# Optimization experiments

Measured on AMD Instinct MI355X. Metric: run time of the kernel, lower is better.

## Reference

```python
import jax, jax.numpy as jnp
import numpy as np

BETA = 0.2
ALPHA_NEG = 0.8
ALPHA_POS = 0.2
EPS = 1e-8  # torch cosine_similarity eps

B, D, P = 8192, 256, 4096


def setup_inputs() -> dict:
    key = jax.random.key(0)
    k1, k2 = jax.random.split(key)
    embeddings = jax.random.normal(k1, (B, D), dtype=jnp.float32)
    positive_pairs = jax.random.randint(k2, (P, 2), 0, B, dtype=jnp.int32)
    return {"embeddings": embeddings, "positive_pairs": positive_pairs}


def reference(embeddings, positive_pairs):
    b = embeddings.shape[0]
    p = positive_pairs.shape[0]
    # cosine similarity matrix (normalize once, single GEMM)
    nrm = jnp.maximum(jnp.linalg.norm(embeddings, axis=1, keepdims=True), EPS)
    e = embeddings / nrm
    cos = e @ e.T                              # [B, B]
    exp_cos = jnp.exp(cos / BETA)
    ii = positive_pairs[:, 0]
    jj = positive_pairs[:, 1]
    # mask = eye + positive pairs (both directions)
    mask = jnp.eye(b, dtype=bool)
    mask = mask.at[ii, jj].set(True).at[jj, ii].set(True)
    exp_masked = jnp.where(mask, 0.0, exp_cos)  # masked_fill(mask, 0)
    pos_ij = exp_cos[ii, jj]                   # [P]
    pos_ji = exp_cos[jj, ii]                   # [P]
    exp_i = exp_masked[ii]                     # [P, B]
    exp_j = exp_masked[jj]                     # [P, B]
    # hard-negative mining via alpha_neg quantile per row
    thr_i = jnp.quantile(exp_i, ALPHA_NEG, axis=1, keepdims=True)
    thr_j = jnp.quantile(exp_j, ALPHA_NEG, axis=1, keepdims=True)
    S_i = jnp.sum(jnp.where(exp_i >= thr_i, exp_i, 0.0), axis=1)  # [P]
    S_j = jnp.sum(jnp.where(exp_j >= thr_j, exp_j, 0.0), axis=1)  # [P]
    # hard-positive mining via alpha_pos quantile
    thr_pij = jnp.quantile(pos_ij, ALPHA_POS)
    thr_pji = jnp.quantile(pos_ji, ALPHA_POS)
    sel_ij = pos_ij <= thr_pij
    sel_ji = pos_ji <= thr_pji
    # torch loop zips the two (order-preserving) boolean-selected lists ->
    # truncates to min count; values are never cross-coupled, only the count.
    kmin = jnp.minimum(sel_ij.sum(), sel_ji.sum())
    act_ij = sel_ij & ((jnp.cumsum(sel_ij.astype(jnp.int32)) - 1) < kmin)
    act_ji = sel_ji & ((jnp.cumsum(sel_ji.astype(jnp.int32)) - 1) < kmin)
    # -log(pk / (pk + S[m])) = log1p(S[m] / pk), summed over all m per pk
    term_ij = jnp.log1p(S_i[None, :] / pos_ij[:, None])  # [P, P]
    term_ji = jnp.log1p(S_j[None, :] / pos_ji[:, None])  # [P, P]
    loss = (jnp.sum(term_ij * act_ij[:, None].astype(term_ij.dtype))
            + jnp.sum(term_ji * act_ji[:, None].astype(term_ji.dtype)))
    return loss / (2.0 * p)
```

## Files before the change

### kernel.cpp

```cpp
#include <hip/hip_runtime.h>
#include <stdint.h>

#define BN    8192
#define DK    256
#define PN    4096
#define MAXP  16
#define HBASE 0x340
#define RANK_ASC 6553

typedef __bf16  bf16_8 __attribute__((ext_vector_type(8)));
typedef __bf16  bf16_4 __attribute__((ext_vector_type(4)));
typedef float   f32x4  __attribute__((ext_vector_type(4)));

__device__ __forceinline__ void gload_lds16(const void* g, void* l) {
  __builtin_amdgcn_global_load_lds(
      (const __attribute__((address_space(1))) unsigned int*)g,
      (__attribute__((address_space(3))) unsigned int*)l, 16, 0, 0);
}

__global__ void prep_clear_kernel(int* pcount, int* rowlist, int* cnt, float* acc) {
  const int i = blockIdx.x * 256 + threadIdx.x;
  if (i < BN) { pcount[i] = 0; rowlist[i] = 0; }
  if (i < 8) acc[i] = 0.f;
  if (i == 0) cnt[0] = 0;
}

__global__ void prep_pairs_kernel(const int2* __restrict__ pairs,
                                  int* pcount, int* partners) {
  const int p = blockIdx.x * 256 + threadIdx.x;
  if (p >= PN) return;
  int2 pr = pairs[p];
  int ix = atomicAdd(&pcount[pr.x], 1);
  if (ix < MAXP) partners[pr.x * MAXP + ix] = pr.y;
  int iy = atomicAdd(&pcount[pr.y], 1);
  if (iy < MAXP) partners[pr.y * MAXP + iy] = pr.x;
}

__global__ void prep_compact_kernel(const int* __restrict__ pcount,
                                    int* rowlist, int* cnt) {
  const int i = blockIdx.x * 256 + threadIdx.x;
  if (i < BN && pcount[i] > 0) {
    int pos = atomicAdd(cnt, 1);
    rowlist[pos] = i;
  }
}

__global__ void __launch_bounds__(256) normalize_kernel(
    const float* __restrict__ X, float* __restrict__ E, __bf16* __restrict__ Ebf) {
  const int tid  = threadIdx.x;
  const int lane = tid & 63;
  const int w    = tid >> 6;
  const int row  = blockIdx.x * 4 + w;
  float4 x = ((const float4*)(X + (size_t)row * DK))[lane];
  float ss = x.x * x.x + x.y * x.y + x.z * x.z + x.w * x.w;
  #pragma unroll
  for (int o = 32; o; o >>= 1) ss += __shfl_xor(ss, o);
  float nrm = fmaxf(sqrtf(ss), 1e-8f);
  float4 e;
  e.x = x.x / nrm; e.y = x.y / nrm; e.z = x.z / nrm; e.w = x.w / nrm;
  ((float4*)(E + (size_t)row * DK))[lane] = e;
  bf16_4 b;
  b[0] = (__bf16)e.x; b[1] = (__bf16)e.y; b[2] = (__bf16)e.z; b[3] = (__bf16)e.w;
  *(bf16_4*)(Ebf + (size_t)row * DK + lane * 4) = b;
}

__global__ void __launch_bounds__(256) pos_kernel(
    const float* __restrict__ E, const int2* __restrict__ pairs, float* __restrict__ pos) {
  const int tid  = threadIdx.x;
  const int lane = tid & 63;
  const int w    = tid >> 6;
  const int p    = blockIdx.x * 4 + w;
  int2 pr = pairs[p];
  float4 a = ((const float4*)(E + (size_t)pr.x * DK))[lane];
  float4 b = ((const float4*)(E + (size_t)pr.y * DK))[lane];
  float d = a.x * b.x + a.y * b.y + a.z * b.z + a.w * b.w;
  #pragma unroll
  for (int o = 32; o; o >>= 1) d += __shfl_xor(d, o);
  if (lane == 0) pos[p] = __expf(5.0f * d);
}

__device__ __forceinline__ void find_bin_256(const unsigned* hist, int rank,
                                             int* sh, unsigned* wtot) {
  const int tid = threadIdx.x, lane = tid & 63, w = tid >> 6;
  unsigned x = hist[tid];
  unsigned pref = x;
  #pragma unroll
  for (int o = 1; o < 64; o <<= 1) {
    unsigned y = __shfl_up(pref, o);
    if (lane >= o) pref += y;
  }
  if (lane == 63) wtot[w] = pref;
  __syncthreads();
  unsigned woff = 0;
  for (int i = 0; i < w; ++i) woff += wtot[i];
  unsigned incl = pref + woff, excl = incl - x;
  if ((unsigned)rank >= excl && (unsigned)rank < incl) { sh[0] = tid; sh[1] = rank - (int)excl; }
  __syncthreads();
}

__global__ void __launch_bounds__(256) pos_thr_kernel(
    const float* __restrict__ pos, float* __restrict__ thr_out) {
  __shared__ uint32_t v[PN];
  __shared__ unsigned hist[256];
  __shared__ int sh[2];
  __shared__ unsigned wtot[4];
  const int tid = threadIdx.x;
  for (int i = tid; i < PN; i += 256) v[i] = ((const uint32_t*)pos)[i];
  __syncthreads();
  int rank = 819;
  uint32_t prefix = 0;
  for (int pass = 0; pass < 4; ++pass) {
    const int shift = 24 - pass * 8;
    hist[tid] = 0;
    __syncthreads();
    for (int i = tid; i < PN; i += 256) {
      uint32_t x = v[i];
      bool match = (pass == 0) || ((x >> (shift + 8)) == (prefix >> (shift + 8)));
      if (match) atomicAdd(&hist[(x >> shift) & 255u], 1u);
    }
    __syncthreads();
    find_bin_256(hist, rank, sh, wtot);
    prefix |= ((uint32_t)sh[0]) << shift;
    rank = sh[1];
    __syncthreads();
  }
  if (tid == 0) {
    float f;
    __builtin_memcpy(&f, &prefix, 4);
    thr_out[0] = f;
  }
}

__global__ void __launch_bounds__(256) gemm_exp_kernel(
    const __bf16* __restrict__ E, const int* __restrict__ rowlist,
    const int* __restrict__ countp, _Float16* __restrict__ out) {
  if ((int)blockIdx.y * 128 >= *countp) return;
  __shared__ __align__(16) __bf16 sA[128 * 32];
  __shared__ __align__(16) __bf16 sB[128 * 32];
  const int tid  = threadIdx.x;
  const int lane = tid & 63;
  const int w    = tid >> 6;
  const int wm   = w >> 1, wn = w & 1;
  const int trow = blockIdx.y * 128;
  const int tcol = blockIdx.x * 128;
  const int r0   = tid >> 2;
  const int seg  = tid & 3;

  const int ga0 = rowlist[trow + r0];
  const int ga1 = rowlist[trow + 64 + r0];
  const __bf16* pa0 = E + (size_t)ga0 * DK + seg * 8;
  const __bf16* pa1 = E + (size_t)ga1 * DK + seg * 8;
  const __bf16* pb0 = E + (size_t)(tcol + r0) * DK + seg * 8;
  const __bf16* pb1 = E + (size_t)(tcol + 64 + r0) * DK + seg * 8;
  __bf16* la0 = &sA[tid * 8];
  __bf16* la1 = &sA[2048 + tid * 8];
  __bf16* lb0 = &sB[tid * 8];
  __bf16* lb1 = &sB[2048 + tid * 8];

  f32x4 acc[4][4];
  #pragma unroll
  for (int i = 0; i < 4; ++i)
    #pragma unroll
    for (int j = 0; j < 4; ++j) {
      f32x4 z = {0.f, 0.f, 0.f, 0.f};
      acc[i][j] = z;
    }

  for (int kt = 0; kt < 8; ++kt) {
    const int k0 = kt * 32;
    __syncthreads();
    gload_lds16(pa0 + k0, la0);
    gload_lds16(pa1 + k0, la1);
    gload_lds16(pb0 + k0, lb0);
    gload_lds16(pb1 + k0, lb1);
    __syncthreads();
    bf16_8 af[4], bfg[4];
    #pragma unroll
    for (int t = 0; t < 4; ++t) {
      af[t]  = *(const bf16_8*)&sA[(wm * 64 + t * 16 + (lane & 15)) * 32 + (lane >> 4) * 8];
      bfg[t] = *(const bf16_8*)&sB[(wn * 64 + t * 16 + (lane & 15)) * 32 + (lane >> 4) * 8];
    }
    #pragma unroll
    for (int i = 0; i < 4; ++i)
      #pragma unroll
      for (int j = 0; j < 4; ++j)
        acc[i][j] = __builtin_amdgcn_mfma_f32_16x16x32_bf16(af[i], bfg[j], acc[i][j], 0, 0, 0);
  }

  const int crow = trow + wm * 64 + (lane >> 4) * 4;
  const int ccol = tcol + wn * 64 + (lane & 15);
  #pragma unroll
  for (int i = 0; i < 4; ++i)
    #pragma unroll
    for (int j = 0; j < 4; ++j)
      #pragma unroll
      for (int r = 0; r < 4; ++r) {
        const int row = crow + i * 16 + r;
        const int col = ccol + j * 16;
        out[(size_t)row * BN + col] = (_Float16)__expf(acc[i][j][r] * 5.0f);
      }
}

__global__ void __launch_bounds__(256) row_stats_kernel(
    const _Float16* __restrict__ expmat, const int* __restrict__ rowlist,
    const int* __restrict__ countp, const int* __restrict__ pcount,
    const int* __restrict__ partners, float* __restrict__ S) {
  __shared__ unsigned hist[4][256];
  __shared__ unsigned total[256];
  __shared__ int plist[MAXP + 1];
  __shared__ int sh[2];
  __shared__ unsigned wtot[4];
  __shared__ float redf[2][4];
  __shared__ unsigned redc[4];
  const int rloc = blockIdx.x;
  if (rloc >= *countp) return;
  const int grow = rowlist[rloc];
  const int tid = threadIdx.x, lane = tid & 63, w = tid >> 6;

  uint4 rv[4];
  const uint4* src = (const uint4*)(expmat + (size_t)rloc * BN);
  #pragma unroll
  for (int q = 0; q < 4; ++q) rv[q] = src[q * 256 + tid];

  int np = pcount[grow]; if (np > MAXP) np = MAXP;
  if (tid < np) plist[tid] = partners[grow * MAXP + tid];
  if (tid == np) plist[tid] = grow;
  ((unsigned*)hist)[tid]       = 0;
  ((unsigned*)hist)[tid + 256] = 0;
  ((unsigned*)hist)[tid + 512] = 0;
  ((unsigned*)hist)[tid + 768] = 0;
  __syncthreads();

  unsigned short hv[32];
  #pragma unroll
  for (int q = 0; q < 4; ++q) {
    union { uint4 u; unsigned short s[8]; } cv;
    cv.u = rv[q];
    #pragma unroll
    for (int j = 0; j < 8; ++j) hv[q * 8 + j] = cv.s[j];
  }

  for (int e = 0; e <= np; ++e) {
    int c = plist[e];
    if (((c >> 3) & 255) == tid) hv[((c >> 11) << 3) | (c & 7)] = 0;
  }

  unsigned* h = hist[w];
  #pragma unroll
  for (int e = 0; e < 32; ++e) {
    int bb = (int)(hv[e] >> 4) - HBASE;
    bb = bb < 0 ? 0 : (bb > 255 ? 255 : bb);
    atomicAdd(&h[bb], 1u);
  }
  __syncthreads();
  total[tid] = hist[0][tid] + hist[1][tid] + hist[2][tid] + hist[3][tid];
  __syncthreads();
  find_bin_256(total, RANK_ASC, sh, wtot);
  const int b    = sh[0];
  const int need = (int)total[b] - sh[1];

  float shi = 0.f, sin_ = 0.f; unsigned cin = 0;
  #pragma unroll
  for (int e = 0; e < 32; ++e) {
    unsigned short x = hv[e];
    int bb = (int)(x >> 4) - HBASE;
    bb = bb < 0 ? 0 : (bb > 255 ? 255 : bb);
    _Float16 hf; __builtin_memcpy(&hf, &x, 2);
    float v = (float)hf;
    if (bb > b) shi += v;
    else if (bb == b) { sin_ += v; cin++; }
  }
  #pragma unroll
  for (int o = 32; o; o >>= 1) {
    shi  += __shfl_xor(shi, o);
    sin_ += __shfl_xor(sin_, o);
    cin  += __shfl_xor(cin, o);
  }
  if (lane == 0) { redf[0][w] = shi; redf[1][w] = sin_; redc[w] = cin; }
  __syncthreads();
  if (tid == 0) {
    float SHI = redf[0][0] + redf[0][1] + redf[0][2] + redf[0][3];
    float SIN = redf[1][0] + redf[1][1] + redf[1][2] + redf[1][3];
    float CIN = (float)(redc[0] + redc[1] + redc[2] + redc[3]);
    S[grow] = SHI + (float)need * (SIN / CIN);
  }
}

__global__ void __launch_bounds__(256) pair_terms_kernel(
    const int2* __restrict__ pairs, const float* __restrict__ S,
    float* __restrict__ acc) {
  __shared__ float red[3][4];
  const int tid = threadIdx.x, lane = tid & 63, w = tid >> 6;
  float t = 0.f, u = 0.f, v = 0.f;
  for (int c = tid; c < PN; c += 256) {
    int2 pr = pairs[c];
    float s1 = S[pr.x], s2 = S[pr.y];
    float i1 = 1.f / s1, i2 = 1.f / s2;
    t += __logf(s1) + __logf(s2);
    u += i1 + i2;
    v += i1 * i1 + i2 * i2;
  }
  #pragma unroll
  for (int o = 32; o; o >>= 1) {
    t += __shfl_xor(t, o); u += __shfl_xor(u, o); v += __shfl_xor(v, o);
  }
  if (lane == 0) { red[0][w] = t; red[1][w] = u; red[2][w] = v; }
  __syncthreads();
  if (tid == 0) {
    acc[0] = red[0][0] + red[0][1] + red[0][2] + red[0][3];
    acc[1] = red[1][0] + red[1][1] + red[1][2] + red[1][3];
    acc[2] = red[2][0] + red[2][1] + red[2][2] + red[2][3];
  }
}

__global__ void __launch_bounds__(256) active_sums_kernel(
    const float* __restrict__ pos, const float* __restrict__ thr_p,
    float* __restrict__ acc) {
  __shared__ float red[4][4];
  const int tid = threadIdx.x, lane = tid & 63, w = tid >> 6;
  const float thr = thr_p[0];
  float n = 0.f, sl = 0.f, sp = 0.f, sp2 = 0.f;
  for (int r = tid; r < PN; r += 256) {
    float p = pos[r];
    if (p <= thr) { n += 1.f; sl += __logf(p); sp += p; sp2 += p * p; }
  }
  #pragma unroll
  for (int o = 32; o; o >>= 1) {
    n += __shfl_xor(n, o); sl += __shfl_xor(sl, o);
    sp += __shfl_xor(sp, o); sp2 += __shfl_xor(sp2, o);
  }
  if (lane == 0) { red[0][w] = n; red[1][w] = sl; red[2][w] = sp; red[3][w] = sp2; }
  __syncthreads();
  if (tid == 0) {
    acc[3] = red[0][0] + red[0][1] + red[0][2] + red[0][3];
    acc[4] = red[1][0] + red[1][1] + red[1][2] + red[1][3];
    acc[5] = red[2][0] + red[2][1] + red[2][2] + red[2][3];
    acc[6] = red[3][0] + red[3][1] + red[3][2] + red[3][3];
  }
}

__global__ void final_loss_kernel(const float* __restrict__ acc, float* __restrict__ out) {
  double T = acc[0], U = acc[1], V = acc[2];
  double n = acc[3], sl = acc[4], sp = acc[5], sp2 = acc[6];
  double num = n * T - 2.0 * (double)PN * sl + sp * U - 0.5 * sp2 * V;
  out[0] = (float)(num / (2.0 * (double)PN));
}

extern "C" void kernel_launch(void* const* d_in, const int* in_sizes, int n_in,
                              void* d_out, int out_size, void* d_ws, size_t ws_size,
                              hipStream_t stream) {
  const float* emb  = (const float*)d_in[0];
  const int2* pairs = (const int2*)d_in[1];
  float* out = (float*)d_out;

  char* w = (char*)d_ws;
  size_t off = 0;
  float*    E     = (float*)(w + off);    off += (size_t)BN * DK * 4;
  __bf16*   Ebf   = (__bf16*)(w + off);   off += (size_t)BN * DK * 2;
  float*    S     = (float*)(w + off);    off += (size_t)BN * 4;
  float*    pos   = (float*)(w + off);    off += (size_t)PN * 4;
  float*    thrp  = (float*)(w + off);    off += 256;
  float*    acc   = (float*)(w + off);    off += 256;
  int*      pcnt  = (int*)(w + off);      off += (size_t)BN * 4;
  int*      parts = (int*)(w + off);      off += (size_t)BN * MAXP * 4;
  int*      rlist = (int*)(w + off);      off += (size_t)BN * 4;
  int*      cnt   = (int*)(w + off);      off += 256;
  _Float16* expc  = (_Float16*)(w + off); off += (size_t)BN * BN * 2;

  prep_clear_kernel<<<BN / 256, 256, 0, stream>>>(pcnt, rlist, cnt, acc);
  normalize_kernel<<<BN / 4, 256, 0, stream>>>(emb, E, Ebf);
  prep_pairs_kernel<<<PN / 256, 256, 0, stream>>>(pairs, pcnt, parts);
  prep_compact_kernel<<<BN / 256, 256, 0, stream>>>(pcnt, rlist, cnt);
  pos_kernel<<<PN / 4, 256, 0, stream>>>(E, pairs, pos);
  pos_thr_kernel<<<1, 256, 0, stream>>>(pos, thrp);
  gemm_exp_kernel<<<dim3(BN / 128, BN / 128), 256, 0, stream>>>(Ebf, rlist, cnt, expc);
  row_stats_kernel<<<BN, 256, 0, stream>>>(expc, rlist, cnt, pcnt, parts, S);
  pair_terms_kernel<<<1, 256, 0, stream>>>(pairs, S, acc);
  active_sums_kernel<<<1, 256, 0, stream>>>(pos, thrp, acc);
  final_loss_kernel<<<1, 1, 0, stream>>>(acc, out);
}
```

Measured before the change: 171.7 us.

## Store exp matrix as fp8 packed by row groups, histogram directly on bytes

```diff
diff --git a/kernel.cpp b/kernel.cpp
--- a/kernel.cpp
+++ b/kernel.cpp
@@ -5,7 +5,6 @@
 #define DK    256
 #define PN    4096
 #define MAXP  16
-#define HBASE 0x340
 #define RANK_ASC 6553
 
 typedef __bf16  bf16_8 __attribute__((ext_vector_type(8)));
@@ -18,10 +17,9 @@
       (__attribute__((address_space(3))) unsigned int*)l, 16, 0, 0);
 }
 
-__global__ void prep_clear_kernel(int* pcount, int* rowlist, int* cnt, float* acc) {
+__global__ void prep_clear_kernel(int* pcount, int* rowlist, int* cnt) {
   const int i = blockIdx.x * 256 + threadIdx.x;
   if (i < BN) { pcount[i] = 0; rowlist[i] = 0; }
-  if (i < 8) acc[i] = 0.f;
   if (i == 0) cnt[0] = 0;
 }
 
@@ -98,42 +96,9 @@
   __syncthreads();
 }
 
-__global__ void __launch_bounds__(256) pos_thr_kernel(
-    const float* __restrict__ pos, float* __restrict__ thr_out) {
-  __shared__ uint32_t v[PN];
-  __shared__ unsigned hist[256];
-  __shared__ int sh[2];
-  __shared__ unsigned wtot[4];
-  const int tid = threadIdx.x;
-  for (int i = tid; i < PN; i += 256) v[i] = ((const uint32_t*)pos)[i];
-  __syncthreads();
-  int rank = 819;
-  uint32_t prefix = 0;
-  for (int pass = 0; pass < 4; ++pass) {
-    const int shift = 24 - pass * 8;
-    hist[tid] = 0;
-    __syncthreads();
-    for (int i = tid; i < PN; i += 256) {
-      uint32_t x = v[i];
-      bool match = (pass == 0) || ((x >> (shift + 8)) == (prefix >> (shift + 8)));
-      if (match) atomicAdd(&hist[(x >> shift) & 255u], 1u);
-    }
-    __syncthreads();
-    find_bin_256(hist, rank, sh, wtot);
-    prefix |= ((uint32_t)sh[0]) << shift;
-    rank = sh[1];
-    __syncthreads();
-  }
-  if (tid == 0) {
-    float f;
-    __builtin_memcpy(&f, &prefix, 4);
-    thr_out[0] = f;
-  }
-}
-
 __global__ void __launch_bounds__(256) gemm_exp_kernel(
     const __bf16* __restrict__ E, const int* __restrict__ rowlist,
-    const int* __restrict__ countp, _Float16* __restrict__ out) {
+    const int* __restrict__ countp, uint32_t* __restrict__ out4) {
   if ((int)blockIdx.y * 128 >= *countp) return;
   __shared__ __align__(16) __bf16 sA[128 * 32];
   __shared__ __align__(16) __bf16 sB[128 * 32];
@@ -190,160 +155,179 @@
   const int crow = trow + wm * 64 + (lane >> 4) * 4;
   const int ccol = tcol + wn * 64 + (lane & 15);
   #pragma unroll
-  for (int i = 0; i < 4; ++i)
-    #pragma unroll
-    for (int j = 0; j < 4; ++j)
-      #pragma unroll
-      for (int r = 0; r < 4; ++r) {
-        const int row = crow + i * 16 + r;
-        const int col = ccol + j * 16;
-        out[(size_t)row * BN + col] = (_Float16)__expf(acc[i][j][r] * 5.0f);
-      }
-}
-
-__global__ void __launch_bounds__(256) row_stats_kernel(
-    const _Float16* __restrict__ expmat, const int* __restrict__ rowlist,
+  for (int i = 0; i < 4; ++i) {
+    const int gidx = (crow + i * 16) >> 2;
+    #pragma unroll
+    for (int j = 0; j < 4; ++j) {
+      const int col = ccol + j * 16;
+      float e0 = __expf(acc[i][j][0] * 5.0f);
+      float e1 = __expf(acc[i][j][1] * 5.0f);
+      float e2 = __expf(acc[i][j][2] * 5.0f);
+      float e3 = __expf(acc[i][j][3] * 5.0f);
+      int u = __builtin_amdgcn_cvt_pk_fp8_f32(e0, e1, 0, false);
+      u     = __builtin_amdgcn_cvt_pk_fp8_f32(e2, e3, u, true);
+      out4[(size_t)gidx * BN + col] = (uint32_t)u;
+    }
+  }
+}
+
+__global__ void __launch_bounds__(256) row_stats4_kernel(
+    const uint32_t* __restrict__ expc4, const int* __restrict__ rowlist,
     const int* __restrict__ countp, const int* __restrict__ pcount,
     const int* __restrict__ partners, float* __restrict__ S) {
-  __shared__ unsigned hist[4][256];
-  __shared__ unsigned total[256];
-  __shared__ int plist[MAXP + 1];
+  __shared__ unsigned hist[4][4][256];
+  __shared__ unsigned total[4][256];
+  __shared__ int plist[4][MAXP + 1];
+  __shared__ int npl[4];
+  __shared__ int growl[4];
   __shared__ int sh[2];
   __shared__ unsigned wtot[4];
-  __shared__ float redf[2][4];
-  __shared__ unsigned redc[4];
-  const int rloc = blockIdx.x;
-  if (rloc >= *countp) return;
-  const int grow = rowlist[rloc];
+  __shared__ float redf[4];
+  const int g = blockIdx.x;
+  const int cnt = *countp;
+  if (g * 4 >= cnt) return;
   const int tid = threadIdx.x, lane = tid & 63, w = tid >> 6;
 
-  uint4 rv[4];
-  const uint4* src = (const uint4*)(expmat + (size_t)rloc * BN);
-  #pragma unroll
-  for (int q = 0; q < 4; ++q) rv[q] = src[q * 256 + tid];
-
-  int np = pcount[grow]; if (np > MAXP) np = MAXP;
-  if (tid < np) plist[tid] = partners[grow * MAXP + tid];
-  if (tid == np) plist[tid] = grow;
-  ((unsigned*)hist)[tid]       = 0;
-  ((unsigned*)hist)[tid + 256] = 0;
-  ((unsigned*)hist)[tid + 512] = 0;
-  ((unsigned*)hist)[tid + 768] = 0;
-  __syncthreads();
-
-  unsigned short hv[32];
-  #pragma unroll
-  for (int q = 0; q < 4; ++q) {
-    union { uint4 u; unsigned short s[8]; } cv;
-    cv.u = rv[q];
-    #pragma unroll
-    for (int j = 0; j < 8; ++j) hv[q * 8 + j] = cv.s[j];
-  }
-
-  for (int e = 0; e <= np; ++e) {
-    int c = plist[e];
-    if (((c >> 3) & 255) == tid) hv[((c >> 11) << 3) | (c & 7)] = 0;
-  }
-
-  unsigned* h = hist[w];
-  #pragma unroll
-  for (int e = 0; e < 32; ++e) {
-    int bb = (int)(hv[e] >> 4) - HBASE;
-    bb = bb < 0 ? 0 : (bb > 255 ? 255 : bb);
-    atomicAdd(&h[bb], 1u);
-  }
-  __syncthreads();
-  total[tid] = hist[0][tid] + hist[1][tid] + hist[2][tid] + hist[3][tid];
-  __syncthreads();
-  find_bin_256(total, RANK_ASC, sh, wtot);
-  const int b    = sh[0];
-  const int need = (int)total[b] - sh[1];
-
-  float shi = 0.f, sin_ = 0.f; unsigned cin = 0;
-  #pragma unroll
-  for (int e = 0; e < 32; ++e) {
-    unsigned short x = hv[e];
-    int bb = (int)(x >> 4) - HBASE;
-    bb = bb < 0 ? 0 : (bb > 255 ? 255 : bb);
-    _Float16 hf; __builtin_memcpy(&hf, &x, 2);
-    float v = (float)hf;
-    if (bb > b) shi += v;
-    else if (bb == b) { sin_ += v; cin++; }
-  }
-  #pragma unroll
-  for (int o = 32; o; o >>= 1) {
-    shi  += __shfl_xor(shi, o);
-    sin_ += __shfl_xor(sin_, o);
-    cin  += __shfl_xor(cin, o);
-  }
-  if (lane == 0) { redf[0][w] = shi; redf[1][w] = sin_; redc[w] = cin; }
-  __syncthreads();
-  if (tid == 0) {
-    float SHI = redf[0][0] + redf[0][1] + redf[0][2] + redf[0][3];
-    float SIN = redf[1][0] + redf[1][1] + redf[1][2] + redf[1][3];
-    float CIN = (float)(redc[0] + redc[1] + redc[2] + redc[3]);
-    S[grow] = SHI + (float)need * (SIN / CIN);
-  }
-}
-
-__global__ void __launch_bounds__(256) pair_terms_kernel(
-    const int2* __restrict__ pairs, const float* __restrict__ S,
-    float* __restrict__ acc) {
-  __shared__ float red[3][4];
-  const int tid = threadIdx.x, lane = tid & 63, w = tid >> 6;
-  float t = 0.f, u = 0.f, v = 0.f;
+  uint4 rv[8];
+  const uint4* src = (const uint4*)(expc4 + (size_t)g * BN);
+  #pragma unroll
+  for (int q = 0; q < 8; ++q) rv[q] = src[q * 256 + tid];
+
+  if (tid < 4) {
+    int rr = g * 4 + tid;
+    int grow = (rr < cnt) ? rowlist[rr] : -1;
+    growl[tid] = grow;
+    int np = 0;
+    if (grow >= 0) {
+      np = pcount[grow]; if (np > MAXP) np = MAXP;
+      for (int e = 0; e < np; ++e) plist[tid][e] = partners[grow * MAXP + e];
+      plist[tid][np] = grow;
+      np++;
+    }
+    npl[tid] = np;
+  }
+  #pragma unroll
+  for (int k = 0; k < 16; ++k) ((unsigned*)hist)[k * 256 + tid] = 0;
+  __syncthreads();
+
+  #pragma unroll
+  for (int r4 = 0; r4 < 4; ++r4) {
+    const int np = npl[r4];
+    for (int e = 0; e < np; ++e) {
+      int c = plist[r4][e];
+      int t = c >> 2;
+      if ((t & 255) == tid) {
+        unsigned* wp = (unsigned*)&rv[t >> 8];
+        wp[c & 3] &= ~(0xFFu << (r4 * 8));
+      }
+    }
+  }
+
+  unsigned* h = (unsigned*)hist[w];
+  #pragma unroll
+  for (int q = 0; q < 8; ++q) {
+    #pragma unroll
+    for (int word = 0; word < 4; ++word) {
+      unsigned dw = ((const unsigned*)&rv[q])[word];
+      atomicAdd(&h[0 * 256 + (dw & 255u)], 1u);
+      atomicAdd(&h[1 * 256 + ((dw >> 8) & 255u)], 1u);
+      atomicAdd(&h[2 * 256 + ((dw >> 16) & 255u)], 1u);
+      atomicAdd(&h[3 * 256 + (dw >> 24)], 1u);
+    }
+  }
+  __syncthreads();
+  #pragma unroll
+  for (int r4 = 0; r4 < 4; ++r4)
+    total[r4][tid] = hist[0][r4][tid] + hist[1][r4][tid] + hist[2][r4][tid] + hist[3][r4][tid];
+  __syncthreads();
+
+  const int Ee = (tid >> 3) & 15, Mm = tid & 7;
+  const float val = (Ee == 0) ? ldexpf((float)Mm, -9) : ldexpf((float)(8 + Mm), Ee - 10);
+
+  for (int r4 = 0; r4 < 4; ++r4) {
+    find_bin_256(total[r4], RANK_ASC, sh, wtot);
+    const int b    = sh[0];
+    const int need = (int)total[r4][b] - sh[1];
+    float contrib = (tid > b) ? (float)total[r4][tid] * val
+                  : (tid == b) ? (float)need * val : 0.f;
+    #pragma unroll
+    for (int o = 32; o; o >>= 1) contrib += __shfl_xor(contrib, o);
+    __syncthreads();
+    if (lane == 0) redf[w] = contrib;
+    __syncthreads();
+    if (tid == 0 && growl[r4] >= 0)
+      S[growl[r4]] = redf[0] + redf[1] + redf[2] + redf[3];
+    __syncthreads();
+  }
+}
+
+__device__ __forceinline__ float block_sum4(float x, float* red4) {
+  const int lane = threadIdx.x & 63, w = threadIdx.x >> 6;
+  #pragma unroll
+  for (int o = 32; o; o >>= 1) x += __shfl_xor(x, o);
+  __syncthreads();
+  if (lane == 0) red4[w] = x;
+  __syncthreads();
+  return red4[0] + red4[1] + red4[2] + red4[3];
+}
+
+__global__ void __launch_bounds__(256) finale_kernel(
+    const float* __restrict__ pos, const int2* __restrict__ pairs,
+    const float* __restrict__ S, float* __restrict__ out) {
+  __shared__ uint32_t v[PN];
+  __shared__ unsigned hist[256];
+  __shared__ int sh[2];
+  __shared__ unsigned wtot[4];
+  __shared__ float red4[4];
+  const int tid = threadIdx.x;
+  for (int i = tid; i < PN; i += 256) v[i] = ((const uint32_t*)pos)[i];
+  __syncthreads();
+
+  int rank = 819;
+  uint32_t prefix = 0;
+  for (int pass = 0; pass < 4; ++pass) {
+    const int shift = 24 - pass * 8;
+    hist[tid] = 0;
+    __syncthreads();
+    for (int i = tid; i < PN; i += 256) {
+      uint32_t x = v[i];
+      bool match = (pass == 0) || ((x >> (shift + 8)) == (prefix >> (shift + 8)));
+      if (match) atomicAdd(&hist[(x >> shift) & 255u], 1u);
+    }
+    __syncthreads();
+    find_bin_256(hist, rank, sh, wtot);
+    prefix |= ((uint32_t)sh[0]) << shift;
+    rank = sh[1];
+    __syncthreads();
+  }
+  float thr; __builtin_memcpy(&thr, &prefix, 4);
+
+  float n = 0.f, sl = 0.f, sp = 0.f, sp2 = 0.f;
+  for (int r = tid; r < PN; r += 256) {
+    float p; uint32_t b = v[r]; __builtin_memcpy(&p, &b, 4);
+    if (p <= thr) { n += 1.f; sl += __logf(p); sp += p; sp2 += p * p; }
+  }
+  float t = 0.f, u = 0.f, vv = 0.f;
   for (int c = tid; c < PN; c += 256) {
     int2 pr = pairs[c];
     float s1 = S[pr.x], s2 = S[pr.y];
     float i1 = 1.f / s1, i2 = 1.f / s2;
     t += __logf(s1) + __logf(s2);
     u += i1 + i2;
-    v += i1 * i1 + i2 * i2;
-  }
-  #pragma unroll
-  for (int o = 32; o; o >>= 1) {
-    t += __shfl_xor(t, o); u += __shfl_xor(u, o); v += __shfl_xor(v, o);
-  }
-  if (lane == 0) { red[0][w] = t; red[1][w] = u; red[2][w] = v; }
-  __syncthreads();
+    vv += i1 * i1 + i2 * i2;
+  }
+  const float N  = block_sum4(n, red4);
+  const float SL = block_sum4(sl, red4);
+  const float SP = block_sum4(sp, red4);
+  const float SP2= block_sum4(sp2, red4);
+  const float T  = block_sum4(t, red4);
+  const float U  = block_sum4(u, red4);
+  const float V  = block_sum4(vv, red4);
   if (tid == 0) {
-    acc[0] = red[0][0] + red[0][1] + red[0][2] + red[0][3];
-    acc[1] = red[1][0] + red[1][1] + red[1][2] + red[1][3];
-    acc[2] = red[2][0] + red[2][1] + red[2][2] + red[2][3];
-  }
-}
-
-__global__ void __launch_bounds__(256) active_sums_kernel(
-    const float* __restrict__ pos, const float* __restrict__ thr_p,
-    float* __restrict__ acc) {
-  __shared__ float red[4][4];
-  const int tid = threadIdx.x, lane = tid & 63, w = tid >> 6;
-  const float thr = thr_p[0];
-  float n = 0.f, sl = 0.f, sp = 0.f, sp2 = 0.f;
-  for (int r = tid; r < PN; r += 256) {
-    float p = pos[r];
-    if (p <= thr) { n += 1.f; sl += __logf(p); sp += p; sp2 += p * p; }
-  }
-  #pragma unroll
-  for (int o = 32; o; o >>= 1) {
-    n += __shfl_xor(n, o); sl += __shfl_xor(sl, o);
-    sp += __shfl_xor(sp, o); sp2 += __shfl_xor(sp2, o);
-  }
-  if (lane == 0) { red[0][w] = n; red[1][w] = sl; red[2][w] = sp; red[3][w] = sp2; }
-  __syncthreads();
-  if (tid == 0) {
-    acc[3] = red[0][0] + red[0][1] + red[0][2] + red[0][3];
-    acc[4] = red[1][0] + red[1][1] + red[1][2] + red[1][3];
-    acc[5] = red[2][0] + red[2][1] + red[2][2] + red[2][3];
-    acc[6] = red[3][0] + red[3][1] + red[3][2] + red[3][3];
-  }
-}
-
-__global__ void final_loss_kernel(const float* __restrict__ acc, float* __restrict__ out) {
-  double T = acc[0], U = acc[1], V = acc[2];
-  double n = acc[3], sl = acc[4], sp = acc[5], sp2 = acc[6];
-  double num = n * T - 2.0 * (double)PN * sl + sp * U - 0.5 * sp2 * V;
-  out[0] = (float)(num / (2.0 * (double)PN));
+    double num = (double)N * T - 2.0 * (double)PN * (double)SL
+               + (double)SP * U - 0.5 * (double)SP2 * V;
+    out[0] = (float)(num / (2.0 * (double)PN));
+  }
 }
 
 extern "C" void kernel_launch(void* const* d_in, const int* in_sizes, int n_in,
@@ -359,23 +343,18 @@
   __bf16*   Ebf   = (__bf16*)(w + off);   off += (size_t)BN * DK * 2;
   float*    S     = (float*)(w + off);    off += (size_t)BN * 4;
   float*    pos   = (float*)(w + off);    off += (size_t)PN * 4;
-  float*    thrp  = (float*)(w + off);    off += 256;
-  float*    acc   = (float*)(w + off);    off += 256;
   int*      pcnt  = (int*)(w + off);      off += (size_t)BN * 4;
   int*      parts = (int*)(w + off);      off += (size_t)BN * MAXP * 4;
   int*      rlist = (int*)(w + off);      off += (size_t)BN * 4;
   int*      cnt   = (int*)(w + off);      off += 256;
-  _Float16* expc  = (_Float16*)(w + off); off += (size_t)BN * BN * 2;
-
-  prep_clear_kernel<<<BN / 256, 256, 0, stream>>>(pcnt, rlist, cnt, acc);
+  uint32_t* expc4 = (uint32_t*)(w + off); off += (size_t)(BN / 4) * BN * 4;
+
+  prep_clear_kernel<<<BN / 256, 256, 0, stream>>>(pcnt, rlist, cnt);
   normalize_kernel<<<BN / 4, 256, 0, stream>>>(emb, E, Ebf);
   prep_pairs_kernel<<<PN / 256, 256, 0, stream>>>(pairs, pcnt, parts);
   prep_compact_kernel<<<BN / 256, 256, 0, stream>>>(pcnt, rlist, cnt);
   pos_kernel<<<PN / 4, 256, 0, stream>>>(E, pairs, pos);
-  pos_thr_kernel<<<1, 256, 0, stream>>>(pos, thrp);
-  gemm_exp_kernel<<<dim3(BN / 128, BN / 128), 256, 0, stream>>>(Ebf, rlist, cnt, expc);
-  row_stats_kernel<<<BN, 256, 0, stream>>>(expc, rlist, cnt, pcnt, parts, S);
-  pair_terms_kernel<<<1, 256, 0, stream>>>(pairs, S, acc);
-  active_sums_kernel<<<1, 256, 0, stream>>>(pos, thrp, acc);
-  final_loss_kernel<<<1, 1, 0, stream>>>(acc, out);
-}
+  gemm_exp_kernel<<<dim3(BN / 128, BN / 128), 256, 0, stream>>>(Ebf, rlist, cnt, expc4);
+  row_stats4_kernel<<<BN / 4, 256, 0, stream>>>(expc4, rlist, cnt, pcnt, parts, S);
+  finale_kernel<<<1, 256, 0, stream>>>(pos, pairs, S, out);
+}
```

After: 177.3 us. 1.03x slower.
